# Kernel optimization log

Measured on AMD Instinct MI355X. Metric: run time of the kernel, lower is better.

## Reference

```python
import jax, jax.numpy as jnp
import numpy as np

EPS = 1e-05  # matches tf entropy epsilon


def setup_inputs() -> dict:
    key = jax.random.key(0)
    k1, k2 = jax.random.split(key)
    encodings = jax.random.normal(k1, (8192, 64), dtype=jnp.float32)
    categorical = jax.random.uniform(k2, (8192, 25), dtype=jnp.float32)
    return {"encodings": encodings, "categorical": categorical, "k": 15}


def reference(encodings, categorical, k):
    B = encodings.shape[0]
    n_components = categorical.shape[1]
    k = min(k, B // 4)  # layer clamps k to batch_size // 4

    hard_groups = jnp.argmax(categorical, axis=1)           # [B] int
    max_groups = jnp.max(categorical, axis=1)               # [B]

    # Batched brute-force kNN. tf.norm's sqrt is monotonic, so the strict
    # comparison `dist < kth_dist` is identical on squared distances; working
    # in squared space avoids sqrt(0) issues and an extra pass.
    sq = jnp.sum(encodings * encodings, axis=1)             # [B]
    d2 = sq[:, None] + sq[None, :] - 2.0 * (encodings @ encodings.T)
    d2 = jnp.maximum(d2, 0.0)                               # [B, B]

    # (k+1)-smallest distances per row (0-indexed k, self-distance included,
    # matching tf.gather(tf.sort(distances), k)).
    neg_topk, _ = jax.lax.top_k(-d2, k + 1)                 # [B, k+1]
    kth = -neg_topk[:, k]                                   # [B] k-th smallest

    mask = (d2 < kth[:, None]).astype(jnp.float32)          # [B, B] strict <

    # Per-row label histogram over the neighborhood: counts[i,c] = #neighbors
    # of i in cluster c. Zero bins contribute 0 to -sum(b*log(b+eps)), same as
    # tf.bincount's variable-length output.
    onehot = jax.nn.one_hot(hard_groups, n_components, dtype=jnp.float32)
    counts = mask @ onehot                                  # [B, n_components]
    n_i = jnp.sum(counts, axis=-1, keepdims=True)           # [B, 1]
    bins = counts / jnp.maximum(n_i, 1.0)
    neighbourhood_entropy = -jnp.sum(bins * jnp.log(bins + EPS), axis=-1)  # [B]

    # Global cluster-size entropy + number of populated clusters.
    gcounts = jnp.sum(onehot, axis=0)                       # [n_components]
    gbins = gcounts / jnp.float32(B)
    cluster_size_entropy = -jnp.sum(gbins * jnp.log(gbins + EPS))
    n_populated = jnp.sum(gcounts > 0).astype(jnp.float32)

    return encodings, neighbourhood_entropy, cluster_size_entropy, n_populated, max_groups
```

## Files before the change

### kernel.cpp

```cpp
#include <hip/hip_runtime.h>
#include <math.h>

#define Bsz    8192
#define Dd     64
#define NC     25
#define RT     16
#define TILES  64
#define KCAP   16
#define EPSf   1e-5f

typedef short  short8  __attribute__((ext_vector_type(8)));
typedef float  floatx4 __attribute__((ext_vector_type(4)));


__device__ inline unsigned short f2bf(float x) {
    unsigned u = __float_as_uint(x);
    u += 0x7FFFu + ((u >> 16) & 1u);
    return (unsigned short)(u >> 16);
}
__device__ inline float bf2f(unsigned short h) { return __uint_as_float(((unsigned)h) << 16); }

__device__ inline void bsort16(unsigned* a) {
    #pragma unroll
    for (int k = 2; k <= 16; k <<= 1)
        #pragma unroll
        for (int j = k >> 1; j > 0; j >>= 1)
            #pragma unroll
            for (int i = 0; i < 16; ++i) {
                int l = i ^ j;
                if (l > i) {
                    bool up = ((i & k) == 0) || (k == 16);
                    unsigned x = a[i], y = a[l];
                    unsigned lo = (x < y) ? x : y, hi = (x < y) ? y : x;
                    a[i] = up ? lo : hi;
                    a[l] = up ? hi : lo;
                }
            }
}
__device__ inline void bclean16(unsigned* t) {
    #pragma unroll
    for (int j = 8; j > 0; j >>= 1)
        #pragma unroll
        for (int i = 0; i < 16; ++i) {
            int l = i ^ j;
            if (l > i) {
                unsigned x = t[i], y = t[l];
                t[i] = (x < y) ? x : y;
                t[l] = (x < y) ? y : x;
            }
        }
}
__device__ inline void bmerge16(unsigned* ls, const unsigned* b) {
    unsigned t[16];
    #pragma unroll
    for (int i = 0; i < 16; ++i) { unsigned x = ls[i], y = b[15 - i]; t[i] = (x < y) ? x : y; }
    bclean16(t);
    #pragma unroll
    for (int i = 0; i < 16; ++i) ls[i] = t[i];
}
__device__ inline void bmerge16_shfl(unsigned* ls, int mask) {
    unsigned t[16];
    #pragma unroll
    for (int i = 0; i < 16; ++i) {
        unsigned pv = (unsigned)__shfl_xor((int)ls[15 - i], mask);
        unsigned x = ls[i];
        t[i] = (x < pv) ? x : pv;
    }
    bclean16(t);
    #pragma unroll
    for (int i = 0; i < 16; ++i) ls[i] = t[i];
}

__device__ inline void compute_pair(
    short8 ah0, short8 ah1, short8 al0, short8 al1,
    short8 ch0, short8 ch1, short8 cl0, short8 cl1,
    uint4 sva, uint4 svb,
    const short8* bh, const short8* bl, float sqi,
    unsigned* cand, int off)
{
    floatx4 accA = (floatx4){0.f, 0.f, 0.f, 0.f};
    floatx4 accB = (floatx4){0.f, 0.f, 0.f, 0.f};
    accA = __builtin_amdgcn_mfma_f32_16x16x32_bf16(ah0, bh[0], accA, 0, 0, 0);
    accB = __builtin_amdgcn_mfma_f32_16x16x32_bf16(ch0, bh[0], accB, 0, 0, 0);
    accA = __builtin_amdgcn_mfma_f32_16x16x32_bf16(ah0, bl[0], accA, 0, 0, 0);
    accB = __builtin_amdgcn_mfma_f32_16x16x32_bf16(ch0, bl[0], accB, 0, 0, 0);
    accA = __builtin_amdgcn_mfma_f32_16x16x32_bf16(al0, bh[0], accA, 0, 0, 0);
    accB = __builtin_amdgcn_mfma_f32_16x16x32_bf16(cl0, bh[0], accB, 0, 0, 0);
    accA = __builtin_amdgcn_mfma_f32_16x16x32_bf16(ah1, bh[1], accA, 0, 0, 0);
    accB = __builtin_amdgcn_mfma_f32_16x16x32_bf16(ch1, bh[1], accB, 0, 0, 0);
    accA = __builtin_amdgcn_mfma_f32_16x16x32_bf16(ah1, bl[1], accA, 0, 0, 0);
    accB = __builtin_amdgcn_mfma_f32_16x16x32_bf16(ch1, bl[1], accB, 0, 0, 0);
    accA = __builtin_amdgcn_mfma_f32_16x16x32_bf16(al1, bh[1], accA, 0, 0, 0);
    accB = __builtin_amdgcn_mfma_f32_16x16x32_bf16(cl1, bh[1], accB, 0, 0, 0);

    unsigned sa[4] = {sva.x, sva.y, sva.z, sva.w};
    unsigned sb[4] = {svb.x, svb.y, svb.z, svb.w};
    #pragma unroll
    for (int r = 0; r < 4; ++r) {
        float d2a = fmaxf(sqi + __uint_as_float(sa[r] & ~31u) + accA[r], 0.f);
        cand[off + r]     = (__float_as_uint(d2a) & ~31u) | (sa[r] & 31u);
        float d2b = fmaxf(sqi + __uint_as_float(sb[r] & ~31u) + accB[r], 0.f);
        cand[off + 4 + r] = (__float_as_uint(d2b) & ~31u) | (sb[r] & 31u);
    }
}


__global__ __launch_bounds__(256) void pre_kernel(
    const float* __restrict__ enc, const float* __restrict__ cat,
    unsigned int* __restrict__ slab,
    char* __restrict__ enc1, char* __restrict__ enc2,
    float* __restrict__ out_max, float* __restrict__ out_enc)
{
    const int tid = threadIdx.x, bid = blockIdx.x;
    const int gid = bid * 256 + tid;

    {
        const float4* src = (const float4*)enc;
        float4* dst = (float4*)out_enc;
        dst[gid] = src[gid];
        dst[gid + 65536] = src[gid + 65536];
    }

    const int w = tid >> 6, lane = tid & 63;
    const int r = lane & 7, s = lane >> 3;
    const int p = bid * 32 + w * 8 + r;
    const int quad = s & 3, kh = s >> 2;
    const int d0 = kh * 32 + quad * 8;

    float4 a = *(const float4*)(enc + p * Dd + d0);
    float4 b = *(const float4*)(enc + p * Dd + d0 + 4);

    float ss = a.x*a.x + a.y*a.y + a.z*a.z + a.w*a.w
             + b.x*b.x + b.y*b.y + b.z*b.z + b.w*b.w;
    ss += __shfl_xor(ss, 8);
    ss += __shfl_xor(ss, 16);
    ss += __shfl_xor(ss, 32);

    {
        float x[8] = {a.x, a.y, a.z, a.w, b.x, b.y, b.z, b.w};
        unsigned h1[4], l1[4], h2[4], l2[4];
        #pragma unroll
        for (int q = 0; q < 4; ++q) {
            unsigned short ha = f2bf(x[2*q]), hb = f2bf(x[2*q+1]);
            unsigned short la = f2bf(x[2*q] - bf2f(ha)), lb = f2bf(x[2*q+1] - bf2f(hb));
            h1[q] = (unsigned)ha | ((unsigned)hb << 16);
            l1[q] = (unsigned)la | ((unsigned)lb << 16);
            float y0 = -2.f * x[2*q], y1 = -2.f * x[2*q+1];
            unsigned short hc = f2bf(y0), hd = f2bf(y1);
            unsigned short lc = f2bf(y0 - bf2f(hc)), ld = f2bf(y1 - bf2f(hd));
            h2[q] = (unsigned)hc | ((unsigned)hd << 16);
            l2[q] = (unsigned)lc | ((unsigned)ld << 16);
        }
        const int g = p >> 4, c15p = p & 15;
        const int base = g * 4096 + kh * 1024 + (quad * 16 + c15p) * 16;
        *(uint4*)(enc1 + base)        = make_uint4(h1[0], h1[1], h1[2], h1[3]);
        *(uint4*)(enc1 + base + 2048) = make_uint4(l1[0], l1[1], l1[2], l1[3]);
        *(uint4*)(enc2 + base)        = make_uint4(h2[0], h2[1], h2[2], h2[3]);
        *(uint4*)(enc2 + base + 2048) = make_uint4(l2[0], l2[1], l2[2], l2[3]);
    }

    float cv = cat[p * NC + s];
    int ci = s;
    #pragma unroll
    for (int t = 1; t < 4; ++t) {
        int idx = s + 8 * t;
        if (idx < NC) {
            float v = cat[p * NC + idx];
            if (v > cv) { cv = v; ci = idx; }
        }
    }
    #pragma unroll
    for (int m = 8; m < 64; m <<= 1) {
        float ov = __shfl_xor(cv, m);
        int   oi = __shfl_xor(ci, m);
        if (ov > cv || (ov == cv && oi < ci)) { cv = ov; ci = oi; }
    }
    if (s == 0) {
        out_max[p] = cv;
        slab[p] = (__float_as_uint(ss) & ~31u) | (unsigned)ci;
    }
}

__global__ __launch_bounds__(512, 4) void main_kernel(
    const char* __restrict__ enc1, const char* __restrict__ enc2,
    const unsigned int* __restrict__ slab, const int* __restrict__ kptr,
    float* __restrict__ out_ent, float* __restrict__ out_glob)
{
    __shared__ unsigned wl[8 * 16 * 17];
    __shared__ int cnt[32];

    const int tid  = threadIdx.x, bid = blockIdx.x;
    const int wv   = tid >> 6, lane = tid & 63;
    const int quad = (tid >> 4) & 3, c15 = tid & 15;
    const int rowbase = bid * RT;

    short8 bh[2], bl[2];
    {
        const char* ib = enc1 + (size_t)bid * 4096 + lane * 16;
        bh[0] = *(const short8*)(ib);
        bh[1] = *(const short8*)(ib + 1024);
        bl[0] = *(const short8*)(ib + 2048);
        bl[1] = *(const short8*)(ib + 3072);
    }
    const float sqi = __uint_as_float(slab[rowbase + c15] & ~31u);

    unsigned ls[KCAP];
    #pragma unroll
    for (int q = 0; q < KCAP; ++q) ls[q] = 0xFFFFFFFFu;
    unsigned cand[16];

    const char* jp = enc2 + (size_t)wv * 4096 + lane * 16;
    const unsigned* sp = slab + wv * 16 + quad * 4;

    short8 Ah0 = *(const short8*)(jp);
    short8 Ah1 = *(const short8*)(jp + 1024);
    short8 Al0 = *(const short8*)(jp + 2048);
    short8 Al1 = *(const short8*)(jp + 3072);
    short8 Ch0 = *(const short8*)(jp + 32768);
    short8 Ch1 = *(const short8*)(jp + 33792);
    short8 Cl0 = *(const short8*)(jp + 34816);
    short8 Cl1 = *(const short8*)(jp + 35840);
    uint4  Asva = *(const uint4*)(sp);
    uint4  Asvb = *(const uint4*)(sp + 128);

    for (int t = 0; t < TILES; t += 4) {
        jp += 65536; sp += 256;
        short8 Bh0 = *(const short8*)(jp);
        short8 Bh1 = *(const short8*)(jp + 1024);
        short8 Bl0 = *(const short8*)(jp + 2048);
        short8 Bl1 = *(const short8*)(jp + 3072);
        short8 Dh0 = *(const short8*)(jp + 32768);
        short8 Dh1 = *(const short8*)(jp + 33792);
        short8 Dl0 = *(const short8*)(jp + 34816);
        short8 Dl1 = *(const short8*)(jp + 35840);
        uint4  Bsva = *(const uint4*)(sp);
        uint4  Bsvb = *(const uint4*)(sp + 128);
        __builtin_amdgcn_sched_barrier(0);
        compute_pair(Ah0, Ah1, Al0, Al1, Ch0, Ch1, Cl0, Cl1, Asva, Asvb,
                     bh, bl, sqi, cand, 0);
        __builtin_amdgcn_sched_barrier(0);
        jp += 65536; sp += 256;
        Ah0 = *(const short8*)(jp);
        Ah1 = *(const short8*)(jp + 1024);
        Al0 = *(const short8*)(jp + 2048);
        Al1 = *(const short8*)(jp + 3072);
        Ch0 = *(const short8*)(jp + 32768);
        Ch1 = *(const short8*)(jp + 33792);
        Cl0 = *(const short8*)(jp + 34816);
        Cl1 = *(const short8*)(jp + 35840);
        Asva = *(const uint4*)(sp);
        Asvb = *(const uint4*)(sp + 128);
        __builtin_amdgcn_sched_barrier(0);
        compute_pair(Bh0, Bh1, Bl0, Bl1, Dh0, Dh1, Dl0, Dl1, Bsva, Bsvb,
                     bh, bl, sqi, cand, 8);
        bsort16(cand);
        bmerge16(ls, cand);
    }

    if (bid == 0) {
        if (tid < 32) cnt[tid] = 0;
        __syncthreads();
        for (int i = tid; i < Bsz; i += 512) atomicAdd(&cnt[slab[i] & 31u], 1);
        __syncthreads();
        if (tid == 0) {
            float gent = 0.f, npop = 0.f;
            for (int i = 0; i < NC; ++i) {
                int g = cnt[i];
                if (g > 0) {
                    npop += 1.f;
                    float gb = (float)g / (float)Bsz;
                    gent -= gb * logf(gb + EPSf);
                }
            }
            out_glob[0] = gent;
            out_glob[1] = npop;
        }
        __syncthreads();
    }

    bmerge16_shfl(ls, 16);
    bmerge16_shfl(ls, 32);
    if (quad == 0) {
        #pragma unroll
        for (int q = 0; q < KCAP; ++q) wl[(wv * 16 + c15) * 17 + q] = ls[q];
    }
    __syncthreads();
    if (wv == 0) {
        const int row = tid >> 2, sub = tid & 3;
        unsigned A[16], Bv[16];
        #pragma unroll
        for (int i = 0; i < 16; ++i) A[i]  = wl[((2 * sub)     * 16 + row) * 17 + i];
        #pragma unroll
        for (int i = 0; i < 16; ++i) Bv[i] = wl[((2 * sub + 1) * 16 + row) * 17 + i];
        bmerge16(A, Bv);
        bmerge16_shfl(A, 1);
        bmerge16_shfl(A, 2);

        int kk = kptr[0];
        if (kk > Bsz / 4) kk = Bsz / 4;
        if (kk > KCAP - 1) kk = KCAP - 1;

        unsigned kth = A[15];
        #pragma unroll
        for (int q = 0; q < 16; ++q) if (q == kk) kth = A[q];
        int nn = 0;
        #pragma unroll
        for (int t = 0; t < 15; ++t) nn += (t < kk && A[t] < kth) ? 1 : 0;

        float inv = 1.f / (float)((nn > 0) ? nn : 1);
        float part = 0.f;
        #pragma unroll
        for (int a4 = 0; a4 < 4; ++a4) {
            int a = sub + 4 * a4;
            if (a < nn) {
                int la = (int)(A[a] & 31u);
                int c = 0;
                #pragma unroll
                for (int b = 0; b < 15; ++b) c += (b < nn && (int)(A[b] & 31u) == la) ? 1 : 0;
                part -= inv * logf((float)c * inv + EPSf);
            }
        }
        part += __shfl_xor(part, 1);
        part += __shfl_xor(part, 2);
        if (sub == 0) out_ent[rowbase + row] = part;
    }
}

extern "C" void kernel_launch(void* const* d_in, const int* in_sizes, int n_in,
                              void* d_out, int out_size, void* d_ws, size_t ws_size,
                              hipStream_t stream)
{
    const float* enc  = (const float*)d_in[0];
    const float* cat  = (const float*)d_in[1];
    const int*   kptr = (const int*)d_in[2];
    float* out = (float*)d_out;

    unsigned int* slab = (unsigned int*)d_ws;
    char*         enc1 = (char*)d_ws + 32768;
    char*         enc2 = (char*)d_ws + 2129920;

    float* out_enc  = out;
    float* out_ent  = out + Bsz * Dd;
    float* out_glob = out + Bsz * Dd + Bsz;
    float* out_max  = out + Bsz * Dd + Bsz + 2;

    pre_kernel<<<256, 256, 0, stream>>>(enc, cat, slab, enc1, enc2, out_max, out);
    main_kernel<<<Bsz / RT, 512, 0, stream>>>(enc1, enc2, slab, kptr, out_ent, out_glob);
}
```

Measured before the change: 123.3 us.

## Stage column tiles through LDS with async global_load_lds double buffering

After: 133.5 us. 1.08x slower.

```diff
diff --git a/kernel.cpp b/kernel.cpp
--- a/kernel.cpp
+++ b/kernel.cpp
@@ -5,13 +5,15 @@
 #define Dd     64
 #define NC     25
 #define RT     16
-#define TILES  64
 #define KCAP   16
 #define EPSf   1e-5f
 
 typedef short  short8  __attribute__((ext_vector_type(8)));
 typedef float  floatx4 __attribute__((ext_vector_type(4)));
 
+
+#define GLD16(g, l) __builtin_amdgcn_global_load_lds((const __attribute__((address_space(1))) unsigned int*)(g), \
+                     (__attribute__((address_space(3))) unsigned int*)(l), 16, 0, 0)
 
 __device__ inline unsigned short f2bf(float x) {
     unsigned u = __float_as_uint(x);
@@ -71,39 +73,6 @@
     for (int i = 0; i < 16; ++i) ls[i] = t[i];
 }
 
-__device__ inline void compute_pair(
-    short8 ah0, short8 ah1, short8 al0, short8 al1,
-    short8 ch0, short8 ch1, short8 cl0, short8 cl1,
-    uint4 sva, uint4 svb,
-    const short8* bh, const short8* bl, float sqi,
-    unsigned* cand, int off)
-{
-    floatx4 accA = (floatx4){0.f, 0.f, 0.f, 0.f};
-    floatx4 accB = (floatx4){0.f, 0.f, 0.f, 0.f};
-    accA = __builtin_amdgcn_mfma_f32_16x16x32_bf16(ah0, bh[0], accA, 0, 0, 0);
-    accB = __builtin_amdgcn_mfma_f32_16x16x32_bf16(ch0, bh[0], accB, 0, 0, 0);
-    accA = __builtin_amdgcn_mfma_f32_16x16x32_bf16(ah0, bl[0], accA, 0, 0, 0);
-    accB = __builtin_amdgcn_mfma_f32_16x16x32_bf16(ch0, bl[0], accB, 0, 0, 0);
-    accA = __builtin_amdgcn_mfma_f32_16x16x32_bf16(al0, bh[0], accA, 0, 0, 0);
-    accB = __builtin_amdgcn_mfma_f32_16x16x32_bf16(cl0, bh[0], accB, 0, 0, 0);
-    accA = __builtin_amdgcn_mfma_f32_16x16x32_bf16(ah1, bh[1], accA, 0, 0, 0);
-    accB = __builtin_amdgcn_mfma_f32_16x16x32_bf16(ch1, bh[1], accB, 0, 0, 0);
-    accA = __builtin_amdgcn_mfma_f32_16x16x32_bf16(ah1, bl[1], accA, 0, 0, 0);
-    accB = __builtin_amdgcn_mfma_f32_16x16x32_bf16(ch1, bl[1], accB, 0, 0, 0);
-    accA = __builtin_amdgcn_mfma_f32_16x16x32_bf16(al1, bh[1], accA, 0, 0, 0);
-    accB = __builtin_amdgcn_mfma_f32_16x16x32_bf16(cl1, bh[1], accB, 0, 0, 0);
-
-    unsigned sa[4] = {sva.x, sva.y, sva.z, sva.w};
-    unsigned sb[4] = {svb.x, svb.y, svb.z, svb.w};
-    #pragma unroll
-    for (int r = 0; r < 4; ++r) {
-        float d2a = fmaxf(sqi + __uint_as_float(sa[r] & ~31u) + accA[r], 0.f);
-        cand[off + r]     = (__float_as_uint(d2a) & ~31u) | (sa[r] & 31u);
-        float d2b = fmaxf(sqi + __uint_as_float(sb[r] & ~31u) + accB[r], 0.f);
-        cand[off + 4 + r] = (__float_as_uint(d2b) & ~31u) | (sb[r] & 31u);
-    }
-}
-
 
 __global__ __launch_bounds__(256) void pre_kernel(
     const float* __restrict__ enc, const float* __restrict__ cat,
@@ -186,8 +155,9 @@
     const unsigned int* __restrict__ slab, const int* __restrict__ kptr,
     float* __restrict__ out_ent, float* __restrict__ out_glob)
 {
-    __shared__ unsigned wl[8 * 16 * 17];
-    __shared__ int cnt[32];
+    __shared__ __align__(16) char stage[8][2][4096];
+    unsigned* wl = (unsigned*)stage;
+    int* cnt = (int*)((char*)stage + 8704);
 
     const int tid  = threadIdx.x, bid = blockIdx.x;
     const int wv   = tid >> 6, lane = tid & 63;
@@ -209,53 +179,65 @@
     for (int q = 0; q < KCAP; ++q) ls[q] = 0xFFFFFFFFu;
     unsigned cand[16];
 
-    const char* jp = enc2 + (size_t)wv * 4096 + lane * 16;
+    __builtin_amdgcn_sched_barrier(0);
+    __builtin_amdgcn_s_waitcnt(0xF70);
+    __builtin_amdgcn_sched_barrier(0);
+    {
+        const char* gsrc = enc2 + (size_t)wv * 4096;
+        char* ldst = (char*)&stage[wv][0][0];
+        #pragma unroll
+        for (int c = 0; c < 4; ++c)
+            GLD16(gsrc + c * 1024 + lane * 16, ldst + c * 1024 + lane * 16);
+    }
     const unsigned* sp = slab + wv * 16 + quad * 4;
 
-    short8 Ah0 = *(const short8*)(jp);
-    short8 Ah1 = *(const short8*)(jp + 1024);
-    short8 Al0 = *(const short8*)(jp + 2048);
-    short8 Al1 = *(const short8*)(jp + 3072);
-    short8 Ch0 = *(const short8*)(jp + 32768);
-    short8 Ch1 = *(const short8*)(jp + 33792);
-    short8 Cl0 = *(const short8*)(jp + 34816);
-    short8 Cl1 = *(const short8*)(jp + 35840);
-    uint4  Asva = *(const uint4*)(sp);
-    uint4  Asvb = *(const uint4*)(sp + 128);
-
-    for (int t = 0; t < TILES; t += 4) {
-        jp += 65536; sp += 256;
-        short8 Bh0 = *(const short8*)(jp);
-        short8 Bh1 = *(const short8*)(jp + 1024);
-        short8 Bl0 = *(const short8*)(jp + 2048);
-        short8 Bl1 = *(const short8*)(jp + 3072);
-        short8 Dh0 = *(const short8*)(jp + 32768);
-        short8 Dh1 = *(const short8*)(jp + 33792);
-        short8 Dl0 = *(const short8*)(jp + 34816);
-        short8 Dl1 = *(const short8*)(jp + 35840);
-        uint4  Bsva = *(const uint4*)(sp);
-        uint4  Bsvb = *(const uint4*)(sp + 128);
+    for (int g = 0; g < 64; ++g) {
+        uint4 sv = *(const uint4*)(sp);
+        sp += 128;
         __builtin_amdgcn_sched_barrier(0);
-        compute_pair(Ah0, Ah1, Al0, Al1, Ch0, Ch1, Cl0, Cl1, Asva, Asvb,
-                     bh, bl, sqi, cand, 0);
+        {
+            int gn = (g + 1) & 63;
+            const char* gsrc = enc2 + ((size_t)(gn * 8 + wv)) * 4096;
+            char* ldst = (char*)&stage[wv][(g + 1) & 1][0];
+            #pragma unroll
+            for (int c = 0; c < 4; ++c)
+                GLD16(gsrc + c * 1024 + lane * 16, ldst + c * 1024 + lane * 16);
+        }
         __builtin_amdgcn_sched_barrier(0);
-        jp += 65536; sp += 256;
-        Ah0 = *(const short8*)(jp);
-        Ah1 = *(const short8*)(jp + 1024);
-        Al0 = *(const short8*)(jp + 2048);
-        Al1 = *(const short8*)(jp + 3072);
-        Ch0 = *(const short8*)(jp + 32768);
-        Ch1 = *(const short8*)(jp + 33792);
-        Cl0 = *(const short8*)(jp + 34816);
-        Cl1 = *(const short8*)(jp + 35840);
-        Asva = *(const uint4*)(sp);
-        Asvb = *(const uint4*)(sp + 128);
+        __builtin_amdgcn_s_waitcnt(0xF75);
         __builtin_amdgcn_sched_barrier(0);
-        compute_pair(Bh0, Bh1, Bl0, Bl1, Dh0, Dh1, Dl0, Dl1, Bsva, Bsvb,
-                     bh, bl, sqi, cand, 8);
-        bsort16(cand);
-        bmerge16(ls, cand);
-    }
+        const char* lb = (const char*)&stage[wv][g & 1][0];
+        short8 ah0 = *(const short8*)(lb + lane * 16);
+        short8 ah1 = *(const short8*)(lb + 1024 + lane * 16);
+        short8 al0 = *(const short8*)(lb + 2048 + lane * 16);
+        short8 al1 = *(const short8*)(lb + 3072 + lane * 16);
+
+        floatx4 acc = (floatx4){0.f, 0.f, 0.f, 0.f};
+        acc = __builtin_amdgcn_mfma_f32_16x16x32_bf16(ah0, bh[0], acc, 0, 0, 0);
+        acc = __builtin_amdgcn_mfma_f32_16x16x32_bf16(ah0, bl[0], acc, 0, 0, 0);
+        acc = __builtin_amdgcn_mfma_f32_16x16x32_bf16(al0, bh[0], acc, 0, 0, 0);
+        acc = __builtin_amdgcn_mfma_f32_16x16x32_bf16(ah1, bh[1], acc, 0, 0, 0);
+        acc = __builtin_amdgcn_mfma_f32_16x16x32_bf16(ah1, bl[1], acc, 0, 0, 0);
+        acc = __builtin_amdgcn_mfma_f32_16x16x32_bf16(al1, bh[1], acc, 0, 0, 0);
+
+        {
+            unsigned sa[4] = {sv.x, sv.y, sv.z, sv.w};
+            #pragma unroll
+            for (int r = 0; r < 4; ++r) {
+                float d2 = fmaxf(sqi + __uint_as_float(sa[r] & ~31u) + acc[r], 0.f);
+                cand[4 * (g & 3) + r] = (__float_as_uint(d2) & ~31u) | (sa[r] & 31u);
+            }
+        }
+        if ((g & 3) == 3) {
+            bsort16(cand);
+            bmerge16(ls, cand);
+        }
+    }
+
+    bmerge16_shfl(ls, 16);
+    bmerge16_shfl(ls, 32);
+
+    __syncthreads();
 
     if (bid == 0) {
         if (tid < 32) cnt[tid] = 0;
@@ -278,8 +260,6 @@
         __syncthreads();
     }
 
-    bmerge16_shfl(ls, 16);
-    bmerge16_shfl(ls, 32);
     if (quad == 0) {
         #pragma unroll
         for (int q = 0; q < KCAP; ++q) wl[(wv * 16 + c15) * 17 + q] = ls[q];
```
